# Kernel tuning notes

Measured on AMD Instinct MI355X. Metric: run time of the kernel, lower is better.

Reference implementation:

```python
import jax, jax.numpy as jnp
import numpy as np

N, T, D_IN, D_OUT = 131072, 16, 128, 128


def setup_inputs() -> dict:
    key = jax.random.key(0)
    k1, k2, k3, k4 = jax.random.split(key, 4)
    x = jax.random.normal(k1, (N, D_IN), dtype=jnp.float32)
    # sorted type ids, matching HeteroLinear(is_sorted=True)
    type_vec = jnp.sort(jax.random.randint(k2, (N,), 0, T)).astype(jnp.int32)
    # HeteroLinear weight: [num_types, in_channels, out_channels]; out = x @ W[t] + b[t]
    weight = (jax.random.normal(k3, (T, D_IN, D_OUT), dtype=jnp.float32)
              / np.float32(np.sqrt(D_IN)))
    bias = jax.random.normal(k4, (T, D_OUT), dtype=jnp.float32) * 0.01
    return {"x": x, "type_vec": type_vec, "weight": weight, "bias": bias}


def _grouped_matmul(x, weight, type_vec):
    """Segment (grouped) matmul: rows are sorted by type; row i uses weight[type_vec[i]]."""
    try:
        # Native grouped-GEMM primitive (exploits is_sorted=True contiguity).
        group_sizes = jnp.bincount(type_vec, length=weight.shape[0]).astype(jnp.int32)
        return jax.lax.ragged_dot(x, weight, group_sizes)
    except Exception:
        # Fallback: small fixed loop over the T types, masked accumulate.
        out = jnp.zeros((x.shape[0], weight.shape[-1]), dtype=x.dtype)
        for t in range(weight.shape[0]):
            out = out + jnp.where((type_vec == t)[:, None], x @ weight[t], jnp.zeros((), x.dtype))
        return out


def reference(x, type_vec, weight, bias):
    # ToHeteroLinear.fused_forward == HeteroLinear(x, type_vec):
    #   out[i] = x[i] @ weight[type_vec[i]] + bias[type_vec[i]]
    out = _grouped_matmul(x, weight, type_vec)  # [N, D_OUT]
    return out + bias[type_vec]
```

## Files before the change

kernel.cpp:

```cpp
#include <hip/hip_runtime.h>

#define DD 128
#define BM 64
#define T_TYPES 16

typedef __bf16 bf16x8 __attribute__((ext_vector_type(8)));
typedef __bf16 bf16x4 __attribute__((ext_vector_type(4)));
typedef float  f32x4  __attribute__((ext_vector_type(4)));

__device__ __forceinline__ void async_copy16(const void* g, void* l) {
    __builtin_amdgcn_global_load_lds(
        (const __attribute__((address_space(1))) unsigned int*)g,
        (__attribute__((address_space(3))) unsigned int*)l, 16, 0, 0);
}

__global__ __launch_bounds__(256) void transpose_w_frag_kernel(
    const float* __restrict__ w, unsigned short* __restrict__ wbf)
{
    __shared__ float lds[DD * 33];
    const int t   = blockIdx.x >> 2;
    const int n0  = (blockIdx.x & 3) * 32;
    const int tid = threadIdx.x;
    const float* wt = w + (size_t)t * DD * DD;

    #pragma unroll
    for (int i = 0; i < 4; ++i) {
        int f = tid + i * 256;
        int k = f >> 3;
        int c = (f & 7) * 4;
        float4 v = *(const float4*)&wt[k * DD + n0 + c];
        lds[k * 33 + c + 0] = v.x;
        lds[k * 33 + c + 1] = v.y;
        lds[k * 33 + c + 2] = v.z;
        lds[k * 33 + c + 3] = v.w;
    }
    __syncthreads();
    #pragma unroll
    for (int i = 0; i < 4; ++i) {
        int g  = tid + i * 256;
        int nl = g >> 5;
        int k4 = (g & 31) * 4;
        int n  = n0 + nl;
        int nt  = n >> 4, n16 = n & 15;
        int kk  = k4 >> 5, q = (k4 >> 3) & 3, jb = k4 & 7;
        int lane = q * 16 + n16;
        size_t ofs = ((((size_t)t * 8 + nt) * 4 + kk) * 64 + lane) * 8 + jb;
        ushort4 o;
        union { __bf16 b; unsigned short u; } cv;
        cv.b = (__bf16)lds[(k4 + 0) * 33 + nl]; o.x = cv.u;
        cv.b = (__bf16)lds[(k4 + 1) * 33 + nl]; o.y = cv.u;
        cv.b = (__bf16)lds[(k4 + 2) * 33 + nl]; o.z = cv.u;
        cv.b = (__bf16)lds[(k4 + 3) * 33 + nl]; o.w = cv.u;
        *(ushort4*)&wbf[ofs] = o;
    }
}

__global__ __launch_bounds__(256, 3) void hetero_main_kernel(
    const float* __restrict__ x,
    const int*   __restrict__ tv,
    const __bf16* __restrict__ wbf,
    const float* __restrict__ bias,
    float*       __restrict__ out)
{
    __shared__ __bf16 As[BM * DD];
    __shared__ __bf16 Bs[DD * DD];

    const int tid  = threadIdx.x;
    const int wave = tid >> 6;
    const int lane = tid & 63;
    const int q    = lane >> 4;
    const int n16  = lane & 15;
    const int row0 = blockIdx.x * BM;

    const int t0 = tv[row0];
    const int t1 = tv[row0 + BM - 1];
    const bool uniform = (t0 == t1);

    {
        const char* gsrc = (const char*)(wbf + (size_t)t0 * DD * DD);
        char* ldst = (char*)Bs;
        const int wbyte = wave * 1024;
        const int gofs  = tid * 16;
        #pragma unroll
        for (int r = 0; r < 8; ++r)
            async_copy16(gsrc + r * 4096 + gofs, ldst + r * 4096 + wbyte);
    }

    {
        const float4* xg = (const float4*)(x + (size_t)row0 * DD);
        #pragma unroll
        for (int i = 0; i < 8; ++i) {
            int f  = tid + i * 256;
            int r  = f >> 5;
            int c4 = (f & 31) << 2;
            float4 v = xg[f];
            bf16x4 pk;
            pk[0] = (__bf16)v.x; pk[1] = (__bf16)v.y;
            pk[2] = (__bf16)v.z; pk[3] = (__bf16)v.w;
            int g = c4 >> 3;
            *(bf16x4*)&As[r * DD + ((g ^ (r & 7)) << 3) + (c4 & 7)] = pk;
        }
    }
    __syncthreads();

    bf16x8 a[4];
    {
        const __bf16* arow = &As[(wave * 16 + n16) * DD];
        #pragma unroll
        for (int kk = 0; kk < 4; ++kk) {
            int gr = ((kk << 2) | q) ^ (n16 & 7);
            a[kk] = *(const bf16x8*)&arow[gr << 3];
        }
    }

    for (int t = t0; t <= t1; ++t) {
        if (t > t0) {
            __syncthreads();
            const char* gsrc = (const char*)(wbf + (size_t)t * DD * DD);
            char* ldst = (char*)Bs;
            const int wbyte = wave * 1024;
            const int gofs  = tid * 16;
            #pragma unroll
            for (int r = 0; r < 8; ++r)
                async_copy16(gsrc + r * 4096 + gofs, ldst + r * 4096 + wbyte);
            __syncthreads();
        }

        f32x4 acc[8];
        #pragma unroll
        for (int nt = 0; nt < 8; ++nt) acc[nt] = (f32x4){0.f, 0.f, 0.f, 0.f};

        #pragma unroll
        for (int nt = 0; nt < 8; ++nt) {
            #pragma unroll
            for (int kk = 0; kk < 4; ++kk) {
                bf16x8 b = *(const bf16x8*)&Bs[(((nt << 2) | kk) << 9) + (lane << 3)];
                acc[nt] = __builtin_amdgcn_mfma_f32_16x16x32_bf16(a[kk], b, acc[nt], 0, 0, 0);
            }
        }

        const int rbase = row0 + wave * 16 + q * 4;
        bool m0 = true, m1 = true, m2 = true, m3 = true;
        if (!uniform) {
            m0 = (tv[rbase + 0] == t);
            m1 = (tv[rbase + 1] == t);
            m2 = (tv[rbase + 2] == t);
            m3 = (tv[rbase + 3] == t);
        }
        #pragma unroll
        for (int nt = 0; nt < 8; ++nt) {
            int   col = nt * 16 + n16;
            float bv  = bias[t * DD + col];
            float* o  = out + (size_t)rbase * DD + col;
            if (m0) o[0 * DD] = acc[nt][0] + bv;
            if (m1) o[1 * DD] = acc[nt][1] + bv;
            if (m2) o[2 * DD] = acc[nt][2] + bv;
            if (m3) o[3 * DD] = acc[nt][3] + bv;
        }
    }
}

extern "C" void kernel_launch(void* const* d_in, const int* in_sizes, int n_in,
                              void* d_out, int out_size, void* d_ws, size_t ws_size,
                              hipStream_t stream) {
    const float* x    = (const float*)d_in[0];
    const int*   tv   = (const int*)d_in[1];
    const float* w    = (const float*)d_in[2];
    const float* bias = (const float*)d_in[3];
    float*       out  = (float*)d_out;
    unsigned short* wbf = (unsigned short*)d_ws;

    int nrows = in_sizes[0] / DD;
    int grid  = nrows / BM;

    hipLaunchKernelGGL(transpose_w_frag_kernel, dim3(T_TYPES * 4), dim3(256), 0, stream,
                       w, wbf);
    hipLaunchKernelGGL(hetero_main_kernel, dim3(grid), dim3(256), 0, stream,
                       x, tv, (const __bf16*)wbf, bias, out);
}
```

Measured before the change: 132.1 us.

## Process four row tiles per block with resident weights and prefetched x

Each block now handles four consecutive 64-row tiles and keeps the current type's bf16 weight tile and bias in LDS and registers, reloading only when the type changes. The next tile's x rows are prefetched into registers while the current tile computes, and each wave owns a private A slice so no block-wide barrier is needed for A. This cuts per-block weight reloads and launch overhead, and hides x load latency. In exchange the grid shrinks fourfold (512 blocks), occupancy drops to 2 blocks per SIMD, and register pressure rises.

```diff
diff --git a/kernel.cpp b/kernel.cpp
--- a/kernel.cpp
+++ b/kernel.cpp
@@ -2,6 +2,7 @@
 
 #define DD 128
 #define BM 64
+#define CHUNK 4
 #define T_TYPES 16
 
 typedef __bf16 bf16x8 __attribute__((ext_vector_type(8)));
@@ -55,14 +56,14 @@
     }
 }
 
-__global__ __launch_bounds__(256, 3) void hetero_main_kernel(
+__global__ __launch_bounds__(256, 2) void hetero_main_kernel(
     const float* __restrict__ x,
     const int*   __restrict__ tv,
     const __bf16* __restrict__ wbf,
     const float* __restrict__ bias,
     float*       __restrict__ out)
 {
-    __shared__ __bf16 As[BM * DD];
+    __shared__ __bf16 As[4 * 16 * DD];
     __shared__ __bf16 Bs[DD * DD];
 
     const int tid  = threadIdx.x;
@@ -70,93 +71,117 @@
     const int lane = tid & 63;
     const int q    = lane >> 4;
     const int n16  = lane & 15;
-    const int row0 = blockIdx.x * BM;
-
-    const int t0 = tv[row0];
-    const int t1 = tv[row0 + BM - 1];
-    const bool uniform = (t0 == t1);
+    const int chunk0 = blockIdx.x * (BM * CHUNK);
+
+    __bf16* Aq = &As[wave * 16 * DD];
+
+    int t_res = tv[chunk0];
 
     {
-        const char* gsrc = (const char*)(wbf + (size_t)t0 * DD * DD);
+        const char* gsrc = (const char*)(wbf + (size_t)t_res * DD * DD);
         char* ldst = (char*)Bs;
-        const int wbyte = wave * 1024;
-        const int gofs  = tid * 16;
+        const int wofs = wave * 1024 + lane * 16;
         #pragma unroll
         for (int r = 0; r < 8; ++r)
-            async_copy16(gsrc + r * 4096 + gofs, ldst + r * 4096 + wbyte);
-    }
-
+            async_copy16(gsrc + r * 4096 + wofs, ldst + r * 4096 + wave * 1024);
+    }
+
+    float bv[8];
+    #pragma unroll
+    for (int nt = 0; nt < 8; ++nt) bv[nt] = bias[t_res * DD + nt * 16 + n16];
+
+    float4 xf[8];
     {
-        const float4* xg = (const float4*)(x + (size_t)row0 * DD);
-        #pragma unroll
-        for (int i = 0; i < 8; ++i) {
-            int f  = tid + i * 256;
+        const float4* p = (const float4*)(x + (size_t)(chunk0 + wave * 16) * DD);
+        #pragma unroll
+        for (int j = 0; j < 8; ++j) xf[j] = p[lane + 64 * j];
+    }
+
+    __syncthreads();
+
+    #pragma unroll
+    for (int tile = 0; tile < CHUNK; ++tile) {
+        const int trow0 = chunk0 + tile * BM;
+        const int wrow0 = trow0 + wave * 16;
+
+        float4 xn[8];
+        if (tile + 1 < CHUNK) {
+            const float4* p = (const float4*)(x + (size_t)(wrow0 + BM) * DD);
+            #pragma unroll
+            for (int j = 0; j < 8; ++j) xn[j] = p[lane + 64 * j];
+        }
+
+        #pragma unroll
+        for (int j = 0; j < 8; ++j) {
+            int f  = lane + 64 * j;
             int r  = f >> 5;
             int c4 = (f & 31) << 2;
-            float4 v = xg[f];
+            int g  = c4 >> 3;
             bf16x4 pk;
-            pk[0] = (__bf16)v.x; pk[1] = (__bf16)v.y;
-            pk[2] = (__bf16)v.z; pk[3] = (__bf16)v.w;
-            int g = c4 >> 3;
-            *(bf16x4*)&As[r * DD + ((g ^ (r & 7)) << 3) + (c4 & 7)] = pk;
-        }
-    }
-    __syncthreads();
-
-    bf16x8 a[4];
-    {
-        const __bf16* arow = &As[(wave * 16 + n16) * DD];
+            pk[0] = (__bf16)xf[j].x; pk[1] = (__bf16)xf[j].y;
+            pk[2] = (__bf16)xf[j].z; pk[3] = (__bf16)xf[j].w;
+            *(bf16x4*)&Aq[r * DD + (((g ^ (r & 7)) << 3) | (c4 & 7))] = pk;
+        }
+
+        bf16x8 a[4];
         #pragma unroll
         for (int kk = 0; kk < 4; ++kk) {
             int gr = ((kk << 2) | q) ^ (n16 & 7);
-            a[kk] = *(const bf16x8*)&arow[gr << 3];
-        }
-    }
-
-    for (int t = t0; t <= t1; ++t) {
-        if (t > t0) {
-            __syncthreads();
-            const char* gsrc = (const char*)(wbf + (size_t)t * DD * DD);
-            char* ldst = (char*)Bs;
-            const int wbyte = wave * 1024;
-            const int gofs  = tid * 16;
-            #pragma unroll
-            for (int r = 0; r < 8; ++r)
-                async_copy16(gsrc + r * 4096 + gofs, ldst + r * 4096 + wbyte);
-            __syncthreads();
-        }
-
-        f32x4 acc[8];
-        #pragma unroll
-        for (int nt = 0; nt < 8; ++nt) acc[nt] = (f32x4){0.f, 0.f, 0.f, 0.f};
-
-        #pragma unroll
-        for (int nt = 0; nt < 8; ++nt) {
-            #pragma unroll
-            for (int kk = 0; kk < 4; ++kk) {
-                bf16x8 b = *(const bf16x8*)&Bs[(((nt << 2) | kk) << 9) + (lane << 3)];
-                acc[nt] = __builtin_amdgcn_mfma_f32_16x16x32_bf16(a[kk], b, acc[nt], 0, 0, 0);
-            }
-        }
-
-        const int rbase = row0 + wave * 16 + q * 4;
-        bool m0 = true, m1 = true, m2 = true, m3 = true;
-        if (!uniform) {
-            m0 = (tv[rbase + 0] == t);
-            m1 = (tv[rbase + 1] == t);
-            m2 = (tv[rbase + 2] == t);
-            m3 = (tv[rbase + 3] == t);
-        }
-        #pragma unroll
-        for (int nt = 0; nt < 8; ++nt) {
-            int   col = nt * 16 + n16;
-            float bv  = bias[t * DD + col];
-            float* o  = out + (size_t)rbase * DD + col;
-            if (m0) o[0 * DD] = acc[nt][0] + bv;
-            if (m1) o[1 * DD] = acc[nt][1] + bv;
-            if (m2) o[2 * DD] = acc[nt][2] + bv;
-            if (m3) o[3 * DD] = acc[nt][3] + bv;
-        }
+            a[kk] = *(const bf16x8*)&Aq[n16 * DD + (gr << 3)];
+        }
+
+        const int tlo = tv[trow0];
+        const int thi = tv[trow0 + BM - 1];
+
+        for (int t = tlo; t <= thi; ++t) {
+            if (t != t_res) {
+                __syncthreads();
+                const char* gsrc = (const char*)(wbf + (size_t)t * DD * DD);
+                char* ldst = (char*)Bs;
+                const int wofs = wave * 1024 + lane * 16;
+                #pragma unroll
+                for (int r = 0; r < 8; ++r)
+                    async_copy16(gsrc + r * 4096 + wofs, ldst + r * 4096 + wave * 1024);
+                t_res = t;
+                #pragma unroll
+                for (int nt = 0; nt < 8; ++nt) bv[nt] = bias[t * DD + nt * 16 + n16];
+                __syncthreads();
+            }
+
+            f32x4 acc[8];
+            #pragma unroll
+            for (int nt = 0; nt < 8; ++nt) acc[nt] = (f32x4){0.f, 0.f, 0.f, 0.f};
+
+            #pragma unroll
+            for (int nt = 0; nt < 8; ++nt) {
+                #pragma unroll
+                for (int kk = 0; kk < 4; ++kk) {
+                    bf16x8 b = *(const bf16x8*)&Bs[(((nt << 2) | kk) << 9) | (lane << 3)];
+                    acc[nt] = __builtin_amdgcn_mfma_f32_16x16x32_bf16(a[kk], b, acc[nt], 0, 0, 0);
+                }
+            }
+
+            const int rbase = wrow0 + q * 4;
+            bool m0 = true, m1 = true, m2 = true, m3 = true;
+            if (tlo != thi) {
+                m0 = (tv[rbase + 0] == t);
+                m1 = (tv[rbase + 1] == t);
+                m2 = (tv[rbase + 2] == t);
+                m3 = (tv[rbase + 3] == t);
+            }
+            float* o = out + (size_t)rbase * DD + n16;
+            #pragma unroll
+            for (int nt = 0; nt < 8; ++nt) {
+                float* oc = o + nt * 16;
+                if (m0) oc[0 * DD] = acc[nt][0] + bv[nt];
+                if (m1) oc[1 * DD] = acc[nt][1] + bv[nt];
+                if (m2) oc[2 * DD] = acc[nt][2] + bv[nt];
+                if (m3) oc[3 * DD] = acc[nt][3] + bv[nt];
+            }
+        }
+
+        #pragma unroll
+        for (int j = 0; j < 8; ++j) xf[j] = xn[j];
     }
 }
 
@@ -171,7 +196,7 @@
     unsigned short* wbf = (unsigned short*)d_ws;
 
     int nrows = in_sizes[0] / DD;
-    int grid  = nrows / BM;
+    int grid  = nrows / (BM * CHUNK);
 
     hipLaunchKernelGGL(transpose_w_frag_kernel, dim3(T_TYPES * 4), dim3(256), 0, stream,
                        w, wbf);
```

Result: faster. 122.5 us (-7.3%).
